# Optimization experiments

Hardware: AMD Instinct MI355X
Metric: run time of the kernel (lower is better)

Reference implementation:

```python
import jax, jax.numpy as jnp
import numpy as np

EPS = 1e-7  # K.epsilon()
NUM_ROUTING = 3

def squash(v, axis=-1):
    s = jnp.sum(jnp.square(v), axis=axis, keepdims=True)
    scale = s / (1.0 + s) / jnp.sqrt(s + EPS)
    return scale * v

def setup_inputs() -> dict:
    key = jax.random.key(0)
    k1, k2 = jax.random.split(key)
    B, J, I = 64, 2048, 16   # batch, input_num_capsule, input_dim_capsule
    K_, D = 32, 16           # num_capsule, dim_capsule
    inputs = jax.random.normal(k1, (B, J, I), dtype=jnp.float32)
    W = jax.random.normal(k2, (K_, J, D, I), dtype=jnp.float32) * 0.05
    return {"inputs": inputs, "W": W}

def reference(inputs, W):
    # inputs: [B, J, I]; W: [K, J, D, I]
    # inputs_hat[b,k,j,d] = sum_i inputs[b,j,i] * W[k,j,d,i]
    u_hat = jnp.einsum('bji,kjdi->bkjd', inputs, W)  # [B,K,J,D]
    B, K_, J, D = u_hat.shape
    b = jnp.zeros((B, K_, J), dtype=u_hat.dtype)
    for i in range(NUM_ROUTING):
        c = jax.nn.softmax(b, axis=1)                # softmax over num_capsule (dim=1)
        s = jnp.einsum('bkj,bkjd->bkd', c, u_hat)    # [B,K,D]
        outputs = squash(s)
        if i < NUM_ROUTING - 1:
            b = b + jnp.einsum('bkd,bkjd->bkj', outputs, u_hat)
    return jnp.concatenate([outputs, c], axis=-1)    # [B, K, D+J]
```

## Files before the change

kernel.cpp:

```cpp
#include <hip/hip_runtime.h>
#include <hip/hip_bf16.h>

#define B_ 64
#define J_ 2048
#define K_ 32
#define D_ 16
#define KD 512
#define NCH 256
#define JCR 8

typedef __attribute__((ext_vector_type(8))) short short8v;
typedef __attribute__((ext_vector_type(16))) float f32x16;

__device__ __forceinline__ float bf2f(unsigned int bits16) {
  unsigned int u = bits16 << 16;
  return __builtin_bit_cast(float, u);
}
__device__ __forceinline__ unsigned int f2bf(float f) {
  unsigned int u = __builtin_bit_cast(unsigned int, f);
  u = u + 0x7fffu + ((u >> 16) & 1u);
  return u >> 16;
}
__device__ __forceinline__ unsigned int cvtpk(float lo, float hi) {
  unsigned int r;
  asm("v_cvt_pk_bf16_f32 %0, %1, %2" : "=v"(r) : "v"(lo), "v"(hi));
  return r;
}
__device__ __forceinline__ f32x16 zero16() {
  f32x16 z;
#pragma unroll
  for (int i = 0; i < 16; ++i) z[i] = 0.f;
  return z;
}

__global__ __launch_bounds__(256) void k_prep(const float* __restrict__ inp,
                                              const float* __restrict__ W,
                                              unsigned short* __restrict__ WB,
                                              unsigned short* __restrict__ XT) {
  const size_t tid = (size_t)blockIdx.x * 256 + threadIdx.x;
  const size_t stride = (size_t)gridDim.x * 256;
  for (size_t g8 = tid; g8 < (size_t)J_ * K_ * 32; g8 += stride) {
    const size_t o = g8 * 8;
    const int j = (int)(o >> 13), k = (int)((o >> 8) & 31), di = (int)(o & 255);
    const float* src = W + ((size_t)k * J_ + j) * 256 + di;
    const float4 a = *(const float4*)src;
    const float4 b = *(const float4*)(src + 4);
    uint4 pk;
    pk.x = cvtpk(a.x, a.y);
    pk.y = cvtpk(a.z, a.w);
    pk.z = cvtpk(b.x, b.y);
    pk.w = cvtpk(b.z, b.w);
    *(uint4*)(WB + o) = pk;
  }
  for (size_t g8 = tid; g8 < (size_t)J_ * B_ * 2; g8 += stride) {
    const size_t o = g8 * 8;
    const int j = (int)(o >> 10), b = (int)((o >> 4) & 63), i0 = (int)(o & 15);
    const float* src = inp + ((size_t)b * J_ + j) * 16 + i0;
    const float4 a = *(const float4*)src;
    const float4 c = *(const float4*)(src + 4);
    uint4 pk;
    pk.x = cvtpk(a.x, a.y);
    pk.y = cvtpk(a.z, a.w);
    pk.z = cvtpk(c.x, c.y);
    pk.w = cvtpk(c.z, c.w);
    *(uint4*)(XT + o) = pk;
  }
}

template <int MODE>
__global__ __launch_bounds__(512, 2) void k_R(const unsigned short* __restrict__ XT,
                                              const unsigned short* __restrict__ WB,
                                              const unsigned short* __restrict__ osB,
                                              unsigned int* __restrict__ spart_pk,
                                              float* __restrict__ cT) {
  const int ch = blockIdx.x;
  const int t = threadIdx.x;
  const int wave = t >> 6, lane = t & 63;
  const int kq = wave & 3, bt = wave >> 2;
  const int hi = lane >> 5, b31 = lane & 31;
  const int b = bt * 32 + b31;
  const int j0 = ch * JCR;

  __shared__ float Sbuf[(MODE >= 1) ? 2 * 4 * 2 * 32 : 4];

  uint4 os_pk[8];
  if constexpr (MODE >= 1) {
    const unsigned short* osb = osB + ((size_t)bt * 64 + lane) * 8 + (size_t)(8 * kq) * 1024;
#pragma unroll
    for (int kk = 0; kk < 8; ++kk) os_pk[kk] = *(const uint4*)(osb + (size_t)kk * 1024);
  }

  float acc[4][16];
#pragma unroll
  for (int q = 0; q < 4; ++q)
#pragma unroll
    for (int s = 0; s < 16; ++s) acc[q][s] = 0.f;

  const unsigned short* waBase =
      WB + (size_t)j0 * 8192 + (b31 >> 4) * 256 + (b31 & 15) * 16 + 8 * hi + (size_t)kq * 2048;
  const unsigned short* xBase = XT + (size_t)j0 * 1024 + b * 16 + 8 * hi;

  uint4 a_cur[4], b_cur;
#pragma unroll
  for (int q = 0; q < 4; ++q) a_cur[q] = *(const uint4*)(waBase + q * 512);
  b_cur = *(const uint4*)(xBase);

  for (int jj = 0; jj < JCR; ++jj) {
    uint4 a_nxt[4], b_nxt;
    if (jj + 1 < JCR) {
#pragma unroll
      for (int q = 0; q < 4; ++q)
        a_nxt[q] = *(const uint4*)(waBase + (size_t)(jj + 1) * 8192 + q * 512);
      b_nxt = *(const uint4*)(xBase + (size_t)(jj + 1) * 1024);
    }

    f32x16 u[4];
#pragma unroll
    for (int q = 0; q < 4; ++q)
      u[q] = __builtin_amdgcn_mfma_f32_32x32x16_bf16(
          __builtin_bit_cast(short8v, a_cur[q]), __builtin_bit_cast(short8v, b_cur),
          zero16(), 0, 0, 0);

    if constexpr (MODE == 0) {
#pragma unroll
      for (int q = 0; q < 4; ++q)
#pragma unroll
        for (int s = 0; s < 16; ++s) acc[q][s] += u[q][s];
    } else {
      float ee[4], eo[4];
      float Sp = 0.f;
#pragma unroll
      for (int q = 0; q < 4; ++q) {
        const unsigned int* o0 = (const unsigned int*)&os_pk[2 * q];
        const unsigned int* o1 = (const unsigned int*)&os_pk[2 * q + 1];
        float pe = 0.f, po = 0.f;
#pragma unroll
        for (int s = 0; s < 8; ++s) {
          const unsigned int w0 = o0[s >> 1], w1 = o1[s >> 1];
          pe = fmaf(u[q][s], bf2f((s & 1) ? (w0 >> 16) : (w0 & 0xffffu)), pe);
          po = fmaf(u[q][8 + s], bf2f((s & 1) ? (w1 >> 16) : (w1 & 0xffffu)), po);
        }
        pe += __shfl_xor(pe, 32);
        po += __shfl_xor(po, 32);
        ee[q] = __expf(pe);
        eo[q] = __expf(po);
        Sp += ee[q] + eo[q];
      }
      if (hi == 0) Sbuf[((jj & 1) * 8 + kq * 2 + bt) * 32 + b31] = Sp;
      __syncthreads();
      const int sb = (jj & 1) * 8;
      const float S = Sbuf[(sb + 0 * 2 + bt) * 32 + b31] + Sbuf[(sb + 1 * 2 + bt) * 32 + b31] +
                      Sbuf[(sb + 2 * 2 + bt) * 32 + b31] + Sbuf[(sb + 3 * 2 + bt) * 32 + b31];
      const float rS = __builtin_amdgcn_rcpf(S);
#pragma unroll
      for (int q = 0; q < 4; ++q) {
        const float ce = ee[q] * rS, co = eo[q] * rS;
#pragma unroll
        for (int s = 0; s < 8; ++s) {
          acc[q][s] = fmaf(ce, u[q][s], acc[q][s]);
          acc[q][8 + s] = fmaf(co, u[q][8 + s], acc[q][8 + s]);
        }
        if constexpr (MODE == 2) {
          if (hi == 0) {
            const int k0 = 8 * kq + 2 * q;
            cT[(size_t)(j0 + jj) * 2048 + (size_t)k0 * 64 + b] = ce;
            cT[(size_t)(j0 + jj) * 2048 + (size_t)(k0 + 1) * 64 + b] = co;
          }
        }
      }
    }
#pragma unroll
    for (int q = 0; q < 4; ++q) a_cur[q] = a_nxt[q];
    b_cur = b_nxt;
  }

  const float sc = (MODE == 0) ? (1.f / 32.f) : 1.f;
#pragma unroll
  for (int q = 0; q < 4; ++q) {
    const int keven = 8 * kq + 2 * q;
    unsigned int* se = spart_pk + (((size_t)b * NCH + ch) * 32 + keven) * 8 + 2 * hi;
    *(uint2*)se = make_uint2(cvtpk(acc[q][0] * sc, acc[q][1] * sc),
                             cvtpk(acc[q][2] * sc, acc[q][3] * sc));
    *(uint2*)(se + 4) = make_uint2(cvtpk(acc[q][4] * sc, acc[q][5] * sc),
                                   cvtpk(acc[q][6] * sc, acc[q][7] * sc));
    unsigned int* so = se + 8;
    *(uint2*)so = make_uint2(cvtpk(acc[q][8] * sc, acc[q][9] * sc),
                             cvtpk(acc[q][10] * sc, acc[q][11] * sc));
    *(uint2*)(so + 4) = make_uint2(cvtpk(acc[q][12] * sc, acc[q][13] * sc),
                                   cvtpk(acc[q][14] * sc, acc[q][15] * sc));
  }
}

__global__ __launch_bounds__(256) void k_cout(const float* __restrict__ cT,
                                              float* __restrict__ outp) {
  const int k = blockIdx.x & 31, j0 = (blockIdx.x >> 5) * 128;
  const int t = threadIdx.x;
  __shared__ float lds[64][129];
#pragma unroll
  for (int m = 0; m < 32; ++m) {
    const int jj = m * 4 + (t >> 6), b = t & 63;
    lds[b][jj] = cT[((size_t)(j0 + jj) * 32 + k) * 64 + b];
  }
  __syncthreads();
#pragma unroll
  for (int m = 0; m < 8; ++m) {
    const int b = m * 8 + (t >> 5), jq = (t & 31) * 4;
    *(float4*)(outp + ((size_t)b * 32 + k) * 2064 + 16 + j0 + jq) =
        make_float4(lds[b][jq], lds[b][jq + 1], lds[b][jq + 2], lds[b][jq + 3]);
  }
}

__global__ __launch_bounds__(256) void k_squash(const unsigned int* __restrict__ spart_pk,
                                                float* __restrict__ osum,
                                                unsigned short* __restrict__ osB,
                                                float* __restrict__ outp,
                                                int first, int final_) {
  const int t = threadIdx.x;
  const int wave = t >> 6, lane = t & 63;
  const int gw = blockIdx.x * 4 + wave;
  const int b = gw >> 5, k = gw & 31;
  const int h = lane & 7, pg = lane >> 3;
  float s0 = 0.f, s1 = 0.f;
#pragma unroll 8
  for (int p = pg; p < NCH; p += 8) {
    const unsigned int v = spart_pk[(((size_t)b * NCH + p) * 32 + k) * 8 + h];
    s0 += bf2f(v & 0xffffu);
    s1 += bf2f(v >> 16);
  }
  s0 += __shfl_xor(s0, 8);  s1 += __shfl_xor(s1, 8);
  s0 += __shfl_xor(s0, 16); s1 += __shfl_xor(s1, 16);
  s0 += __shfl_xor(s0, 32); s1 += __shfl_xor(s1, 32);
  float ss = s0 * s0 + s1 * s1;
  ss += __shfl_xor(ss, 1); ss += __shfl_xor(ss, 2); ss += __shfl_xor(ss, 4);
  const float scale = (ss / (1.f + ss)) * rsqrtf(ss + 1e-7f);
  const float ov0 = scale * s0, ov1 = scale * s1;
  if (final_) {
    if (pg == 0)
      *(float2*)(outp + ((size_t)b * K_ + k) * 2064 + 2 * h) = make_float2(ov0, ov1);
  } else {
    if (pg == 0) {
      float2 prev = make_float2(0.f, 0.f);
      if (!first) prev = *(const float2*)(osum + b * KD + k * 16 + 2 * h);
      const float ns0 = prev.x + ov0, ns1 = prev.y + ov1;
      *(float2*)(osum + b * KD + k * 16 + 2 * h) = make_float2(ns0, ns1);
      const int d0 = 2 * h;
      const int hi0 = (d0 >> 2) & 1;
      const int slot0 = (d0 & 3) + ((d0 >> 3) << 2);
      *(unsigned int*)(osB + (((size_t)k * 2 + (b >> 5)) * 64 + hi0 * 32 + (b & 31)) * 8 +
                       slot0) = cvtpk(ns0, ns1);
    }
  }
}

extern "C" void kernel_launch(void* const* d_in, const int* in_sizes, int n_in,
                              void* d_out, int out_size, void* d_ws, size_t ws_size,
                              hipStream_t stream) {
  const float* inp = (const float*)d_in[0];
  const float* W   = (const float*)d_in[1];
  float* outp = (float*)d_out;
  char* ws = (char*)d_ws;
  unsigned short* WB = (unsigned short*)ws;
  unsigned short* XT = (unsigned short*)(ws + (size_t)33554432);
  float* cT    = (float*)(ws + (size_t)37748736);
  unsigned int* spart_pk = (unsigned int*)(ws + (size_t)54525952);
  float* osum  = (float*)(ws + (size_t)88080384);
  unsigned short* osB = (unsigned short*)(ws + (size_t)88211456);

  k_prep<<<2048, 256, 0, stream>>>(inp, W, WB, XT);
  k_R<0><<<NCH, 512, 0, stream>>>(XT, WB, nullptr, spart_pk, nullptr);
  k_squash<<<B_ * K_ / 4, 256, 0, stream>>>(spart_pk, osum, osB, outp, 1, 0);
  k_R<1><<<NCH, 512, 0, stream>>>(XT, WB, osB, spart_pk, nullptr);
  k_squash<<<B_ * K_ / 4, 256, 0, stream>>>(spart_pk, osum, osB, outp, 0, 0);
  k_R<2><<<NCH, 512, 0, stream>>>(XT, WB, osB, spart_pk, cT);
  k_squash<<<B_ * K_ / 4, 256, 0, stream>>>(spart_pk, osum, osB, outp, 0, 1);
  k_cout<<<K_ * 16, 256, 0, stream>>>(cT, outp);
}
```

Baseline: 95.55 us.

## Fuse W bf16 conversion into first routing pass and c output into last

The separate prep pass that converted W to bf16 is removed. The first routing kernel now reads fp32 W directly, converts it in registers, feeds the MFMA with accumulation, and writes the bf16 copy for later passes. The final routing kernel stages coupling coefficients in LDS and writes them transposed straight into the output, which eliminates the cT buffer and the k_cout kernel. This saves a full memory pass over W and an intermediate round trip. In exchange, W is read redundantly by two wave groups, and the final kernel uses a large LDS footprint that may reduce occupancy.

New measurement: 93.49 us. -2.2%, faster.

```diff
diff --git a/kernel.cpp b/kernel.cpp
--- a/kernel.cpp
+++ b/kernel.cpp
@@ -33,25 +33,10 @@
   return z;
 }
 
-__global__ __launch_bounds__(256) void k_prep(const float* __restrict__ inp,
-                                              const float* __restrict__ W,
-                                              unsigned short* __restrict__ WB,
-                                              unsigned short* __restrict__ XT) {
+__global__ __launch_bounds__(256) void k_prepX(const float* __restrict__ inp,
+                                               unsigned short* __restrict__ XT) {
   const size_t tid = (size_t)blockIdx.x * 256 + threadIdx.x;
   const size_t stride = (size_t)gridDim.x * 256;
-  for (size_t g8 = tid; g8 < (size_t)J_ * K_ * 32; g8 += stride) {
-    const size_t o = g8 * 8;
-    const int j = (int)(o >> 13), k = (int)((o >> 8) & 31), di = (int)(o & 255);
-    const float* src = W + ((size_t)k * J_ + j) * 256 + di;
-    const float4 a = *(const float4*)src;
-    const float4 b = *(const float4*)(src + 4);
-    uint4 pk;
-    pk.x = cvtpk(a.x, a.y);
-    pk.y = cvtpk(a.z, a.w);
-    pk.z = cvtpk(b.x, b.y);
-    pk.w = cvtpk(b.z, b.w);
-    *(uint4*)(WB + o) = pk;
-  }
   for (size_t g8 = tid; g8 < (size_t)J_ * B_ * 2; g8 += stride) {
     const size_t o = g8 * 8;
     const int j = (int)(o >> 10), b = (int)((o >> 4) & 63), i0 = (int)(o & 15);
@@ -67,12 +52,10 @@
   }
 }
 
-template <int MODE>
-__global__ __launch_bounds__(512, 2) void k_R(const unsigned short* __restrict__ XT,
-                                              const unsigned short* __restrict__ WB,
-                                              const unsigned short* __restrict__ osB,
-                                              unsigned int* __restrict__ spart_pk,
-                                              float* __restrict__ cT) {
+__global__ __launch_bounds__(512, 2) void k_R0W(const float* __restrict__ W,
+                                                const unsigned short* __restrict__ XT,
+                                                unsigned short* __restrict__ WB,
+                                                unsigned int* __restrict__ spart_pk) {
   const int ch = blockIdx.x;
   const int t = threadIdx.x;
   const int wave = t >> 6, lane = t & 63;
@@ -81,100 +64,56 @@
   const int b = bt * 32 + b31;
   const int j0 = ch * JCR;
 
-  __shared__ float Sbuf[(MODE >= 1) ? 2 * 4 * 2 * 32 : 4];
-
-  uint4 os_pk[8];
-  if constexpr (MODE >= 1) {
-    const unsigned short* osb = osB + ((size_t)bt * 64 + lane) * 8 + (size_t)(8 * kq) * 1024;
-#pragma unroll
-    for (int kk = 0; kk < 8; ++kk) os_pk[kk] = *(const uint4*)(osb + (size_t)kk * 1024);
-  }
-
-  float acc[4][16];
-#pragma unroll
-  for (int q = 0; q < 4; ++q)
-#pragma unroll
-    for (int s = 0; s < 16; ++s) acc[q][s] = 0.f;
-
-  const unsigned short* waBase =
-      WB + (size_t)j0 * 8192 + (b31 >> 4) * 256 + (b31 & 15) * 16 + 8 * hi + (size_t)kq * 2048;
+  const float* wsrc = W + ((size_t)(8 * kq + (b31 >> 4)) * J_ + j0) * 256 +
+                      (b31 & 15) * 16 + 8 * hi;
+  unsigned short* wdst = WB + (size_t)j0 * 8192 + kq * 2048 + (b31 >> 4) * 256 +
+                         (b31 & 15) * 16 + 8 * hi;
   const unsigned short* xBase = XT + (size_t)j0 * 1024 + b * 16 + 8 * hi;
-
-  uint4 a_cur[4], b_cur;
-#pragma unroll
-  for (int q = 0; q < 4; ++q) a_cur[q] = *(const uint4*)(waBase + q * 512);
-  b_cur = *(const uint4*)(xBase);
+  const size_t qstep = (size_t)2 * J_ * 256;
+
+  f32x16 acc[4];
+#pragma unroll
+  for (int q = 0; q < 4; ++q) acc[q] = zero16();
+
+  float4 wc[8];
+  uint4 xc;
+#pragma unroll
+  for (int q = 0; q < 4; ++q) {
+    wc[2 * q]     = *(const float4*)(wsrc + (size_t)q * qstep);
+    wc[2 * q + 1] = *(const float4*)(wsrc + (size_t)q * qstep + 4);
+  }
+  xc = *(const uint4*)xBase;
 
   for (int jj = 0; jj < JCR; ++jj) {
-    uint4 a_nxt[4], b_nxt;
+    float4 wn[8];
+    uint4 xn;
     if (jj + 1 < JCR) {
 #pragma unroll
-      for (int q = 0; q < 4; ++q)
-        a_nxt[q] = *(const uint4*)(waBase + (size_t)(jj + 1) * 8192 + q * 512);
-      b_nxt = *(const uint4*)(xBase + (size_t)(jj + 1) * 1024);
-    }
-
-    f32x16 u[4];
-#pragma unroll
-    for (int q = 0; q < 4; ++q)
-      u[q] = __builtin_amdgcn_mfma_f32_32x32x16_bf16(
-          __builtin_bit_cast(short8v, a_cur[q]), __builtin_bit_cast(short8v, b_cur),
-          zero16(), 0, 0, 0);
-
-    if constexpr (MODE == 0) {
-#pragma unroll
-      for (int q = 0; q < 4; ++q)
-#pragma unroll
-        for (int s = 0; s < 16; ++s) acc[q][s] += u[q][s];
-    } else {
-      float ee[4], eo[4];
-      float Sp = 0.f;
-#pragma unroll
       for (int q = 0; q < 4; ++q) {
-        const unsigned int* o0 = (const unsigned int*)&os_pk[2 * q];
-        const unsigned int* o1 = (const unsigned int*)&os_pk[2 * q + 1];
-        float pe = 0.f, po = 0.f;
-#pragma unroll
-        for (int s = 0; s < 8; ++s) {
-          const unsigned int w0 = o0[s >> 1], w1 = o1[s >> 1];
-          pe = fmaf(u[q][s], bf2f((s & 1) ? (w0 >> 16) : (w0 & 0xffffu)), pe);
-          po = fmaf(u[q][8 + s], bf2f((s & 1) ? (w1 >> 16) : (w1 & 0xffffu)), po);
-        }
-        pe += __shfl_xor(pe, 32);
-        po += __shfl_xor(po, 32);
-        ee[q] = __expf(pe);
-        eo[q] = __expf(po);
-        Sp += ee[q] + eo[q];
+        const float* ws2 = wsrc + (size_t)(jj + 1) * 256 + (size_t)q * qstep;
+        wn[2 * q] = *(const float4*)ws2;
+        wn[2 * q + 1] = *(const float4*)(ws2 + 4);
       }
-      if (hi == 0) Sbuf[((jj & 1) * 8 + kq * 2 + bt) * 32 + b31] = Sp;
-      __syncthreads();
-      const int sb = (jj & 1) * 8;
-      const float S = Sbuf[(sb + 0 * 2 + bt) * 32 + b31] + Sbuf[(sb + 1 * 2 + bt) * 32 + b31] +
-                      Sbuf[(sb + 2 * 2 + bt) * 32 + b31] + Sbuf[(sb + 3 * 2 + bt) * 32 + b31];
-      const float rS = __builtin_amdgcn_rcpf(S);
-#pragma unroll
-      for (int q = 0; q < 4; ++q) {
-        const float ce = ee[q] * rS, co = eo[q] * rS;
-#pragma unroll
-        for (int s = 0; s < 8; ++s) {
-          acc[q][s] = fmaf(ce, u[q][s], acc[q][s]);
-          acc[q][8 + s] = fmaf(co, u[q][8 + s], acc[q][8 + s]);
-        }
-        if constexpr (MODE == 2) {
-          if (hi == 0) {
-            const int k0 = 8 * kq + 2 * q;
-            cT[(size_t)(j0 + jj) * 2048 + (size_t)k0 * 64 + b] = ce;
-            cT[(size_t)(j0 + jj) * 2048 + (size_t)(k0 + 1) * 64 + b] = co;
-          }
-        }
-      }
-    }
-#pragma unroll
-    for (int q = 0; q < 4; ++q) a_cur[q] = a_nxt[q];
-    b_cur = b_nxt;
-  }
-
-  const float sc = (MODE == 0) ? (1.f / 32.f) : 1.f;
+      xn = *(const uint4*)(xBase + (size_t)(jj + 1) * 1024);
+    }
+    const short8v xf = __builtin_bit_cast(short8v, xc);
+#pragma unroll
+    for (int q = 0; q < 4; ++q) {
+      uint4 wv;
+      wv.x = cvtpk(wc[2 * q].x, wc[2 * q].y);
+      wv.y = cvtpk(wc[2 * q].z, wc[2 * q].w);
+      wv.z = cvtpk(wc[2 * q + 1].x, wc[2 * q + 1].y);
+      wv.w = cvtpk(wc[2 * q + 1].z, wc[2 * q + 1].w);
+      if (bt == 0) *(uint4*)(wdst + (size_t)jj * 8192 + q * 512) = wv;
+      acc[q] = __builtin_amdgcn_mfma_f32_32x32x16_bf16(
+          __builtin_bit_cast(short8v, wv), xf, acc[q], 0, 0, 0);
+    }
+#pragma unroll
+    for (int p = 0; p < 8; ++p) wc[p] = wn[p];
+    xc = xn;
+  }
+
+  const float sc = 1.f / 32.f;
 #pragma unroll
   for (int q = 0; q < 4; ++q) {
     const int keven = 8 * kq + 2 * q;
@@ -191,22 +130,130 @@
   }
 }
 
-__global__ __launch_bounds__(256) void k_cout(const float* __restrict__ cT,
+template <int MODE>
+__global__ __launch_bounds__(512, 2) void k_R(const unsigned short* __restrict__ XT,
+                                              const unsigned short* __restrict__ WB,
+                                              const unsigned short* __restrict__ osB,
+                                              unsigned int* __restrict__ spart_pk,
                                               float* __restrict__ outp) {
-  const int k = blockIdx.x & 31, j0 = (blockIdx.x >> 5) * 128;
+  const int ch = blockIdx.x;
   const int t = threadIdx.x;
-  __shared__ float lds[64][129];
-#pragma unroll
-  for (int m = 0; m < 32; ++m) {
-    const int jj = m * 4 + (t >> 6), b = t & 63;
-    lds[b][jj] = cT[((size_t)(j0 + jj) * 32 + k) * 64 + b];
-  }
-  __syncthreads();
-#pragma unroll
-  for (int m = 0; m < 8; ++m) {
-    const int b = m * 8 + (t >> 5), jq = (t & 31) * 4;
-    *(float4*)(outp + ((size_t)b * 32 + k) * 2064 + 16 + j0 + jq) =
-        make_float4(lds[b][jq], lds[b][jq + 1], lds[b][jq + 2], lds[b][jq + 3]);
+  const int wave = t >> 6, lane = t & 63;
+  const int kq = wave & 3, bt = wave >> 2;
+  const int hi = lane >> 5, b31 = lane & 31;
+  const int b = bt * 32 + b31;
+  const int j0 = ch * JCR;
+
+  __shared__ float Sbuf[2 * 4 * 2 * 32];
+  __shared__ float c_lds[(MODE == 2) ? 32 * 64 * 9 : 4];
+
+  uint4 os_pk[8];
+  {
+    const unsigned short* osb = osB + ((size_t)bt * 64 + lane) * 8 + (size_t)(8 * kq) * 1024;
+#pragma unroll
+    for (int kk = 0; kk < 8; ++kk) os_pk[kk] = *(const uint4*)(osb + (size_t)kk * 1024);
+  }
+
+  float acc[4][16];
+#pragma unroll
+  for (int q = 0; q < 4; ++q)
+#pragma unroll
+    for (int s = 0; s < 16; ++s) acc[q][s] = 0.f;
+
+  const unsigned short* waBase =
+      WB + (size_t)j0 * 8192 + (b31 >> 4) * 256 + (b31 & 15) * 16 + 8 * hi + (size_t)kq * 2048;
+  const unsigned short* xBase = XT + (size_t)j0 * 1024 + b * 16 + 8 * hi;
+
+  uint4 a_cur[4], b_cur;
+#pragma unroll
+  for (int q = 0; q < 4; ++q) a_cur[q] = *(const uint4*)(waBase + q * 512);
+  b_cur = *(const uint4*)(xBase);
+
+  for (int jj = 0; jj < JCR; ++jj) {
+    uint4 a_nxt[4], b_nxt;
+    if (jj + 1 < JCR) {
+#pragma unroll
+      for (int q = 0; q < 4; ++q)
+        a_nxt[q] = *(const uint4*)(waBase + (size_t)(jj + 1) * 8192 + q * 512);
+      b_nxt = *(const uint4*)(xBase + (size_t)(jj + 1) * 1024);
+    }
+
+    f32x16 u[4];
+#pragma unroll
+    for (int q = 0; q < 4; ++q)
+      u[q] = __builtin_amdgcn_mfma_f32_32x32x16_bf16(
+          __builtin_bit_cast(short8v, a_cur[q]), __builtin_bit_cast(short8v, b_cur),
+          zero16(), 0, 0, 0);
+
+    float ee[4], eo[4];
+    float Sp = 0.f;
+#pragma unroll
+    for (int q = 0; q < 4; ++q) {
+      const unsigned int* o0 = (const unsigned int*)&os_pk[2 * q];
+      const unsigned int* o1 = (const unsigned int*)&os_pk[2 * q + 1];
+      float pe = 0.f, po = 0.f;
+#pragma unroll
+      for (int s = 0; s < 8; ++s) {
+        const unsigned int w0 = o0[s >> 1], w1 = o1[s >> 1];
+        pe = fmaf(u[q][s], bf2f((s & 1) ? (w0 >> 16) : (w0 & 0xffffu)), pe);
+        po = fmaf(u[q][8 + s], bf2f((s & 1) ? (w1 >> 16) : (w1 & 0xffffu)), po);
+      }
+      pe += __shfl_xor(pe, 32);
+      po += __shfl_xor(po, 32);
+      ee[q] = __expf(pe);
+      eo[q] = __expf(po);
+      Sp += ee[q] + eo[q];
+    }
+    if (hi == 0) Sbuf[((jj & 1) * 8 + kq * 2 + bt) * 32 + b31] = Sp;
+    __syncthreads();
+    const int sb = (jj & 1) * 8;
+    const float S = Sbuf[(sb + 0 * 2 + bt) * 32 + b31] + Sbuf[(sb + 1 * 2 + bt) * 32 + b31] +
+                    Sbuf[(sb + 2 * 2 + bt) * 32 + b31] + Sbuf[(sb + 3 * 2 + bt) * 32 + b31];
+    const float rS = __builtin_amdgcn_rcpf(S);
+#pragma unroll
+    for (int q = 0; q < 4; ++q) {
+      const float ce = ee[q] * rS, co = eo[q] * rS;
+#pragma unroll
+      for (int s = 0; s < 8; ++s) {
+        acc[q][s] = fmaf(ce, u[q][s], acc[q][s]);
+        acc[q][8 + s] = fmaf(co, u[q][8 + s], acc[q][8 + s]);
+      }
+      if constexpr (MODE == 2) {
+        if (hi == 0) {
+          const int k0 = 8 * kq + 2 * q;
+          c_lds[((k0)*64 + b) * 9 + jj] = ce;
+          c_lds[((k0 + 1) * 64 + b) * 9 + jj] = co;
+        }
+      }
+    }
+#pragma unroll
+    for (int q = 0; q < 4; ++q) a_cur[q] = a_nxt[q];
+    b_cur = b_nxt;
+  }
+
+#pragma unroll
+  for (int q = 0; q < 4; ++q) {
+    const int keven = 8 * kq + 2 * q;
+    unsigned int* se = spart_pk + (((size_t)b * NCH + ch) * 32 + keven) * 8 + 2 * hi;
+    *(uint2*)se = make_uint2(cvtpk(acc[q][0], acc[q][1]), cvtpk(acc[q][2], acc[q][3]));
+    *(uint2*)(se + 4) = make_uint2(cvtpk(acc[q][4], acc[q][5]), cvtpk(acc[q][6], acc[q][7]));
+    unsigned int* so = se + 8;
+    *(uint2*)so = make_uint2(cvtpk(acc[q][8], acc[q][9]), cvtpk(acc[q][10], acc[q][11]));
+    *(uint2*)(so + 4) =
+        make_uint2(cvtpk(acc[q][12], acc[q][13]), cvtpk(acc[q][14], acc[q][15]));
+  }
+
+  if constexpr (MODE == 2) {
+    __syncthreads();
+#pragma unroll
+    for (int m = 0; m < 4; ++m) {
+      const int r = m * 512 + t;
+      const int k = r >> 6, bb = r & 63;
+      const float* cr = &c_lds[r * 9];
+      float* orow = outp + ((size_t)bb * K_ + k) * 2064 + 16 + j0;
+      *(float4*)orow = make_float4(cr[0], cr[1], cr[2], cr[3]);
+      *(float4*)(orow + 4) = make_float4(cr[4], cr[5], cr[6], cr[7]);
+    }
   }
 }
 
@@ -261,17 +308,15 @@
   char* ws = (char*)d_ws;
   unsigned short* WB = (unsigned short*)ws;
   unsigned short* XT = (unsigned short*)(ws + (size_t)33554432);
-  float* cT    = (float*)(ws + (size_t)37748736);
-  unsigned int* spart_pk = (unsigned int*)(ws + (size_t)54525952);
-  float* osum  = (float*)(ws + (size_t)88080384);
-  unsigned short* osB = (unsigned short*)(ws + (size_t)88211456);
-
-  k_prep<<<2048, 256, 0, stream>>>(inp, W, WB, XT);
-  k_R<0><<<NCH, 512, 0, stream>>>(XT, WB, nullptr, spart_pk, nullptr);
+  unsigned int* spart_pk = (unsigned int*)(ws + (size_t)37748736);
+  float* osum  = (float*)(ws + (size_t)54525952);
+  unsigned short* osB = (unsigned short*)(ws + (size_t)54525952 + 131072);
+
+  k_prepX<<<512, 256, 0, stream>>>(inp, XT);
+  k_R0W<<<NCH, 512, 0, stream>>>(W, XT, WB, spart_pk);
   k_squash<<<B_ * K_ / 4, 256, 0, stream>>>(spart_pk, osum, osB, outp, 1, 0);
   k_R<1><<<NCH, 512, 0, stream>>>(XT, WB, osB, spart_pk, nullptr);
   k_squash<<<B_ * K_ / 4, 256, 0, stream>>>(spart_pk, osum, osB, outp, 0, 0);
-  k_R<2><<<NCH, 512, 0, stream>>>(XT, WB, osB, spart_pk, cT);
+  k_R<2><<<NCH, 512, 0, stream>>>(XT, WB, osB, spart_pk, outp);
   k_squash<<<B_ * K_ / 4, 256, 0, stream>>>(spart_pk, osum, osB, outp, 0, 1);
-  k_cout<<<K_ * 16, 256, 0, stream>>>(cT, outp);
-}
+}
```

## Fuse coupling-coefficient output transpose into final routing kernel via LDS

Applied to the files above, without the earlier changes.

The final routing pass now stages the softmax coefficients in a shared-memory tile and writes them straight into the output tensor at the end of each block. This removes the intermediate cT buffer round trip through global memory and the separate transpose kernel launch. In exchange, the MODE 2 kernel uses about 73 KB more LDS, which may cut occupancy below the two blocks per CU requested by its launch bounds. Its output stores are also only 32-byte chunks per row, which coalesce less well.

Measured after the change: 95.71 us. Within noise of the previous version (+0.2%).

```diff
diff --git a/kernel.cpp b/kernel.cpp
--- a/kernel.cpp
+++ b/kernel.cpp
@@ -72,7 +72,7 @@
                                               const unsigned short* __restrict__ WB,
                                               const unsigned short* __restrict__ osB,
                                               unsigned int* __restrict__ spart_pk,
-                                              float* __restrict__ cT) {
+                                              float* __restrict__ outp) {
   const int ch = blockIdx.x;
   const int t = threadIdx.x;
   const int wave = t >> 6, lane = t & 63;
@@ -82,6 +82,7 @@
   const int j0 = ch * JCR;
 
   __shared__ float Sbuf[(MODE >= 1) ? 2 * 4 * 2 * 32 : 4];
+  __shared__ float c_lds[(MODE == 2) ? 32 * 64 * 9 : 4];
 
   uint4 os_pk[8];
   if constexpr (MODE >= 1) {
@@ -163,8 +164,8 @@
         if constexpr (MODE == 2) {
           if (hi == 0) {
             const int k0 = 8 * kq + 2 * q;
-            cT[(size_t)(j0 + jj) * 2048 + (size_t)k0 * 64 + b] = ce;
-            cT[(size_t)(j0 + jj) * 2048 + (size_t)(k0 + 1) * 64 + b] = co;
+            c_lds[((k0)*64 + b) * 9 + jj] = ce;
+            c_lds[((k0 + 1) * 64 + b) * 9 + jj] = co;
           }
         }
       }
@@ -189,24 +190,18 @@
     *(uint2*)(so + 4) = make_uint2(cvtpk(acc[q][12] * sc, acc[q][13] * sc),
                                    cvtpk(acc[q][14] * sc, acc[q][15] * sc));
   }
-}
-
-__global__ __launch_bounds__(256) void k_cout(const float* __restrict__ cT,
-                                              float* __restrict__ outp) {
-  const int k = blockIdx.x & 31, j0 = (blockIdx.x >> 5) * 128;
-  const int t = threadIdx.x;
-  __shared__ float lds[64][129];
-#pragma unroll
-  for (int m = 0; m < 32; ++m) {
-    const int jj = m * 4 + (t >> 6), b = t & 63;
-    lds[b][jj] = cT[((size_t)(j0 + jj) * 32 + k) * 64 + b];
-  }
-  __syncthreads();
-#pragma unroll
-  for (int m = 0; m < 8; ++m) {
-    const int b = m * 8 + (t >> 5), jq = (t & 31) * 4;
-    *(float4*)(outp + ((size_t)b * 32 + k) * 2064 + 16 + j0 + jq) =
-        make_float4(lds[b][jq], lds[b][jq + 1], lds[b][jq + 2], lds[b][jq + 3]);
+
+  if constexpr (MODE == 2) {
+    __syncthreads();
+#pragma unroll
+    for (int m = 0; m < 4; ++m) {
+      const int r = m * 512 + t;
+      const int k = r >> 6, bb = r & 63;
+      const float* cr = &c_lds[r * 9];
+      float* orow = outp + ((size_t)bb * K_ + k) * 2064 + 16 + j0;
+      *(float4*)orow = make_float4(cr[0], cr[1], cr[2], cr[3]);
+      *(float4*)(orow + 4) = make_float4(cr[4], cr[5], cr[6], cr[7]);
+    }
   }
 }
 
@@ -261,17 +256,15 @@
   char* ws = (char*)d_ws;
   unsigned short* WB = (unsigned short*)ws;
   unsigned short* XT = (unsigned short*)(ws + (size_t)33554432);
-  float* cT    = (float*)(ws + (size_t)37748736);
-  unsigned int* spart_pk = (unsigned int*)(ws + (size_t)54525952);
-  float* osum  = (float*)(ws + (size_t)88080384);
-  unsigned short* osB = (unsigned short*)(ws + (size_t)88211456);
+  unsigned int* spart_pk = (unsigned int*)(ws + (size_t)37748736);
+  float* osum  = (float*)(ws + (size_t)54525952);
+  unsigned short* osB = (unsigned short*)(ws + (size_t)54525952 + 131072);
 
   k_prep<<<2048, 256, 0, stream>>>(inp, W, WB, XT);
   k_R<0><<<NCH, 512, 0, stream>>>(XT, WB, nullptr, spart_pk, nullptr);
   k_squash<<<B_ * K_ / 4, 256, 0, stream>>>(spart_pk, osum, osB, outp, 1, 0);
   k_R<1><<<NCH, 512, 0, stream>>>(XT, WB, osB, spart_pk, nullptr);
   k_squash<<<B_ * K_ / 4, 256, 0, stream>>>(spart_pk, osum, osB, outp, 0, 0);
-  k_R<2><<<NCH, 512, 0, stream>>>(XT, WB, osB, spart_pk, cT);
+  k_R<2><<<NCH, 512, 0, stream>>>(XT, WB, osB, spart_pk, outp);
   k_squash<<<B_ * K_ / 4, 256, 0, stream>>>(spart_pk, osum, osB, outp, 0, 1);
-  k_cout<<<K_ * 16, 256, 0, stream>>>(cT, outp);
-}
+}
```
